# Kernel tuning notes

Hardware: AMD Instinct MI355X
Metric: run time of the kernel (lower is better)

## Reference

```python
import jax, jax.numpy as jnp
import numpy as np

B, S, E = 4, 2048, 1024
H, DK = 16, 64

def setup_inputs() -> dict:
    key = jax.random.key(0)
    ks = jax.random.split(key, 9)
    sc = 1.0 / np.sqrt(E)
    return {
        "q": jax.random.normal(ks[0], (B, S, E), jnp.float32),
        "Wq": jax.random.normal(ks[1], (E, H * DK), jnp.float32) * sc,
        "bq": jax.random.normal(ks[2], (H * DK,), jnp.float32) * 0.01,
        "Wk": jax.random.normal(ks[3], (E, H * DK), jnp.float32) * sc,
        "bk": jax.random.normal(ks[4], (H * DK,), jnp.float32) * 0.01,
        "Wv": jax.random.normal(ks[5], (E, H * DK), jnp.float32) * sc,
        "bv": jax.random.normal(ks[6], (H * DK,), jnp.float32) * 0.01,
        "Wo": jax.random.normal(ks[7], (H * DK, E), jnp.float32) * sc,
        "bo": jax.random.normal(ks[8], (E,), jnp.float32) * 0.01,
    }

def _split_heads(x):
    # (B, S, H*DK) -> (B, H, S, DK)
    return x.reshape(B, S, H, DK).transpose(0, 2, 1, 3)

def reference(q, Wq, bq, Wk, bk, Wv, bv, Wo, bo):
    # self-attention: k = v = q (torch module path when k=v=None)
    qh = _split_heads(q @ Wq + bq)
    kh = _split_heads(q @ Wk + bk)
    vh = _split_heads(q @ Wv + bv)
    scale = 1.0 / jnp.sqrt(jnp.asarray(DK, qh.dtype))
    scores = jnp.einsum("bhqd,bhkd->bhqk", qh, kh) * scale  # (B,H,S,S)
    attn = jax.nn.softmax(scores, axis=-1)
    ctx = jnp.einsum("bhqk,bhkd->bhqd", attn, vh)
    ctx = ctx.transpose(0, 2, 1, 3).reshape(B, S, H * DK)
    return ctx @ Wo + bo
```

## Files before the change

kernel.cpp:

```cpp
#include <hip/hip_runtime.h>
#include <hip/hip_bf16.h>
#include <math.h>


typedef _Float16 f16x8 __attribute__((ext_vector_type(8)));
typedef _Float16 f16x4 __attribute__((ext_vector_type(4)));
typedef _Float16 f16x2 __attribute__((ext_vector_type(2)));
typedef float    f32x4 __attribute__((ext_vector_type(4)));

#define MFMA16(a,b,c) __builtin_amdgcn_mfma_f32_16x16x32_f16(a,b,c,0,0,0)

__device__ __forceinline__ void async_cp16(const _Float16* g, _Float16* l) {
    __builtin_amdgcn_global_load_lds(
        (const __attribute__((address_space(1))) unsigned int*)g,
        (__attribute__((address_space(3))) unsigned int*)l,
        16, 0, 0);
}

__device__ __forceinline__ f16x2 pk(float a, float b) {
    return __builtin_bit_cast(f16x2, __builtin_amdgcn_cvt_pkrtz(a, b));
}

__global__ void __launch_bounds__(256) prep_weights(
    const float* __restrict__ Wq, const float* __restrict__ Wk,
    const float* __restrict__ Wv, const float* __restrict__ Wo,
    _Float16* __restrict__ wt)
{
    __shared__ float tile[32][33];
    int mat = blockIdx.y;
    const float* W = (mat==0)?Wq:(mat==1)?Wk:(mat==2)?Wv:Wo;
    _Float16* WT = wt + (size_t)mat*1048576;
    int t = blockIdx.x;
    int kb = (t & 31) * 32;
    int nb = (t >> 5) * 32;
    int tx = threadIdx.x & 31, ty = threadIdx.x >> 5;
    #pragma unroll
    for (int r = 0; r < 4; ++r) {
        int row = ty + r*8;
        tile[row][tx] = W[(size_t)(kb+row)*1024 + nb + tx];
    }
    __syncthreads();
    #pragma unroll
    for (int r = 0; r < 4; ++r) {
        int row = ty + r*8;
        WT[(size_t)(nb+row)*1024 + kb + tx] = (_Float16)tile[tx][row];
    }
}

__global__ void __launch_bounds__(256) cvt_x(
    const float* __restrict__ X, _Float16* __restrict__ Xh)
{
    int i = (blockIdx.x*256 + threadIdx.x)*4;
    f32x4 x = *(const f32x4*)&X[i];
    f16x4 h;
    #pragma unroll
    for (int k=0;k<4;k++) h[k] = (_Float16)x[k];
    *(f16x4*)&Xh[i] = h;
}

__global__ void __launch_bounds__(256) gemm_qkv(
    const _Float16* __restrict__ Xh, const _Float16* __restrict__ wt,
    const float* __restrict__ bq, const float* __restrict__ bk, const float* __restrict__ bv,
    _Float16* __restrict__ Q, _Float16* __restrict__ K, _Float16* __restrict__ Vt)
{
    __shared__ __align__(16) _Float16 sA[8192];
    __shared__ __align__(16) _Float16 sB[8192];

    const int id = blockIdx.x;
    const int msub = id & 7;
    const int t2 = id >> 3;
    const int nblk = t2 % 24;
    const int mblk = (t2 / 24) * 8 + msub;

    const int tid = threadIdx.x;
    const int wave = tid >> 6, lane = tid & 63;
    const int wr = wave >> 1, wc = wave & 1;
    const int q4 = lane >> 4, cc = lane & 15;

    const int mat = nblk >> 3;
    const int colbase = (nblk & 7) * 128;
    const _Float16* Bg = wt + (size_t)mat*1048576 + (size_t)colbase*1024;
    const _Float16* Ag = Xh + (size_t)mblk*131072;

    f32x4 acc[4][4] = {};

    const int srow = tid >> 3;
    const int scg  = ((tid & 7) ^ ((tid >> 3) & 7)) * 8;

    for (int kb = 0; kb < 1024; kb += 64) {
        __syncthreads();
        #pragma unroll
        for (int rr = 0; rr < 4; ++rr) {
            async_cp16(&Ag[(size_t)(rr*32 + srow)*1024 + kb + scg], sA + rr*2048 + wave*512);
            async_cp16(&Bg[(size_t)(rr*32 + srow)*1024 + kb + scg], sB + rr*2048 + wave*512);
        }
        __syncthreads();
        #pragma unroll
        for (int ks = 0; ks < 2; ++ks) {
            f16x8 af[4], bf[4];
            #pragma unroll
            for (int i=0;i<4;i++){
                af[i] = *(const f16x8*)&sA[(wr*64+i*16+cc)*64 + ((ks*4+q4)^(cc&7))*8];
                bf[i] = *(const f16x8*)&sB[(wc*64+i*16+cc)*64 + ((ks*4+q4)^(cc&7))*8];
            }
            #pragma unroll
            for (int i=0;i<4;i++)
                #pragma unroll
                for (int j=0;j<4;j++)
                    acc[i][j] = MFMA16(af[i], bf[j], acc[i][j]);
        }
    }

    const float* bias = (mat==0)?bq:(mat==1)?bk:bv;
    const float QSCALE = 0.125f * 1.44269504f;
    #pragma unroll
    for (int i=0;i<4;i++)
      #pragma unroll
      for (int j=0;j<4;j++)
        #pragma unroll
        for (int r=0;r<4;r++){
            int m = mblk*128 + wr*64 + i*16 + q4*4 + r;
            int ncol = colbase + wc*64 + j*16 + cc;
            float val = acc[i][j][r] + bias[ncol];
            int b = m >> 11, s = m & 2047;
            int h = ncol >> 6, dk = ncol & 63;
            if (mat == 2) {
                Vt[((size_t)(b*16+h)*64 + dk)*2048 + s] = (_Float16)val;
            } else {
                size_t qi = ((size_t)(b*16+h)*2048 + s)*64 + dk;
                if (mat == 0) Q[qi] = (_Float16)(val * QSCALE);
                else          K[qi] = (_Float16)val;
            }
        }
}

__global__ void __launch_bounds__(256,2) attn(
    const _Float16* __restrict__ Qg, const _Float16* __restrict__ Kg,
    const _Float16* __restrict__ Vg,
    _Float16* __restrict__ Ctx)
{
    __shared__ __align__(16) _Float16 sK[128][72];
    __shared__ __align__(16) _Float16 sV[64][136];
    __shared__ __align__(16) _Float16 sP[128*128];

    const int id = blockIdx.x;
    const int xcd = id & 7;
    const int t2 = id >> 3;
    const int qc = t2 & 15;
    const int bh = (t2 >> 4) * 8 + xcd;

    const int tid = threadIdx.x;
    const int wave = tid >> 6, lane = tid & 63;
    const int q4 = lane >> 4, cc = lane & 15;

    const size_t hoff = (size_t)bh * 131072;
    const _Float16* Qp = Qg + hoff;
    const _Float16* Kp = Kg + hoff;
    const _Float16* Vp = Vg + hoff;

    const int qbase = qc*128 + wave*32;

    f16x8 qf[2][2];
    #pragma unroll
    for (int m=0;m<2;m++)
      #pragma unroll
      for (int ks=0;ks<2;ks++)
        qf[m][ks] = *(const f16x8*)&Qp[(qbase+m*16+cc)*64 + ks*32 + q4*8];

    f16x8 vones;
    #pragma unroll
    for (int k=0;k<8;k++) vones[k] = (_Float16)1.0f;

    f32x4 o[2][4] = {};
    f32x4 oL[2] = {};

    const int r0 = tid >> 3, c8 = (tid & 7)*8;
    const int vrow = tid >> 4, vg = (tid & 15)*8;

    const int prow_w0 = wave*32 + cc;

    f16x8 kr[4], vr[4];
    #pragma unroll
    for (int p=0;p<4;p++){
        kr[p] = *(const f16x8*)&Kp[(p*32 + r0)*64 + c8];
        vr[p] = *(const f16x8*)&Vp[(size_t)(p*16 + vrow)*2048 + vg];
    }

    for (int kt = 0; kt < 16; ++kt) {
        __syncthreads();
        #pragma unroll
        for (int p=0;p<4;p++){
            *(f16x8*)&sK[p*32+r0][c8] = kr[p];
            *(f16x8*)&sV[p*16+vrow][vg] = vr[p];
        }
        __syncthreads();
        if (kt < 15) {
            #pragma unroll
            for (int p=0;p<4;p++){
                kr[p] = *(const f16x8*)&Kp[((kt+1)*128 + p*32 + r0)*64 + c8];
                vr[p] = *(const f16x8*)&Vp[(size_t)(p*16 + vrow)*2048 + (kt+1)*128 + vg];
            }
        }

        #pragma unroll
        for (int kj=0;kj<8;kj++){
            f16x8 k0 = *(const f16x8*)&sK[kj*16+cc][q4*8];
            f16x8 k1 = *(const f16x8*)&sK[kj*16+cc][32+q4*8];
            #pragma unroll
            for (int m=0;m<2;m++){
                f32x4 z = {};
                f32x4 s = MFMA16(k0, qf[m][0], z);
                s = MFMA16(k1, qf[m][1], s);
                float p0 = __builtin_amdgcn_exp2f(s[0]);
                float p1 = __builtin_amdgcn_exp2f(s[1]);
                float p2 = __builtin_amdgcn_exp2f(s[2]);
                float p3 = __builtin_amdgcn_exp2f(s[3]);
                union { f16x4 v4; f16x2 v2[2]; } u;
                u.v2[0] = pk(p0, p1);
                u.v2[1] = pk(p2, p3);
                int row = prow_w0 + m*16;
                int g   = (kj*2 + (q4>>1)) ^ (row & 7);
                *(f16x4*)&sP[row*128 + g*8 + (q4&1)*4] = u.v4;
            }
        }

        #pragma unroll
        for (int ks=0;ks<4;ks++){
            int g0 = ks*4 + q4;
            int row0 = prow_w0;
            int row1 = prow_w0 + 16;
            f16x8 p0 = *(const f16x8*)&sP[row0*128 + (g0 ^ (row0 & 7))*8];
            f16x8 p1 = *(const f16x8*)&sP[row1*128 + (g0 ^ (row1 & 7))*8];
            #pragma unroll
            for (int v=0;v<4;v++){
                f16x8 vf = *(const f16x8*)&sV[v*16+cc][ks*32+q4*8];
                o[0][v] = MFMA16(p0, vf, o[0][v]);
                o[1][v] = MFMA16(p1, vf, o[1][v]);
            }
            oL[0] = MFMA16(p0, vones, oL[0]);
            oL[1] = MFMA16(p1, vones, oL[1]);
        }
    }

    int b = bh >> 4, h = bh & 15;
    #pragma unroll
    for (int m=0;m<2;m++)
      #pragma unroll
      for (int r=0;r<4;r++){
        float inv = 1.f / oL[m][r];
        int s = qbase + m*16 + q4*4 + r;
        #pragma unroll
        for (int v=0;v<4;v++){
            float val = o[m][v][r]*inv;
            int dk = v*16 + cc;
            Ctx[((size_t)(b*2048+s)*16 + h)*64 + dk] = (_Float16)val;
        }
      }
}

__global__ void __launch_bounds__(256) gemm_out(
    const _Float16* __restrict__ Ctx, const _Float16* __restrict__ wt,
    const float* __restrict__ bo,
    float* __restrict__ out)
{
    __shared__ __align__(16) _Float16 sA[8192];
    __shared__ __align__(16) _Float16 sB[8192];

    const int id = blockIdx.x;
    const int msub = id & 7;
    const int t2 = id >> 3;
    const int nblk = t2 & 7;
    const int mblk = (t2 >> 3) * 8 + msub;

    const int tid = threadIdx.x;
    const int wave = tid >> 6, lane = tid & 63;
    const int wr = wave >> 1, wc = wave & 1;
    const int q4 = lane >> 4, cc = lane & 15;

    const _Float16* Bg = wt + (size_t)3*1048576 + (size_t)nblk*128*1024;
    const _Float16* Ag = Ctx + (size_t)mblk*131072;

    f32x4 acc[4][4] = {};
    const int srow = tid >> 3;
    const int scg  = ((tid & 7) ^ ((tid >> 3) & 7)) * 8;

    for (int kb = 0; kb < 1024; kb += 64) {
        __syncthreads();
        #pragma unroll
        for (int rr = 0; rr < 4; ++rr) {
            async_cp16(&Ag[(size_t)(rr*32 + srow)*1024 + kb + scg], sA + rr*2048 + wave*512);
            async_cp16(&Bg[(size_t)(rr*32 + srow)*1024 + kb + scg], sB + rr*2048 + wave*512);
        }
        __syncthreads();
        #pragma unroll
        for (int ks = 0; ks < 2; ++ks) {
            f16x8 af[4], bf[4];
            #pragma unroll
            for (int i=0;i<4;i++){
                af[i] = *(const f16x8*)&sA[(wr*64+i*16+cc)*64 + ((ks*4+q4)^(cc&7))*8];
                bf[i] = *(const f16x8*)&sB[(wc*64+i*16+cc)*64 + ((ks*4+q4)^(cc&7))*8];
            }
            #pragma unroll
            for (int i=0;i<4;i++)
                #pragma unroll
                for (int j=0;j<4;j++)
                    acc[i][j] = MFMA16(af[i], bf[j], acc[i][j]);
        }
    }

    #pragma unroll
    for (int i=0;i<4;i++)
      #pragma unroll
      for (int j=0;j<4;j++)
        #pragma unroll
        for (int r=0;r<4;r++){
            int m = mblk*128 + wr*64 + i*16 + q4*4 + r;
            int n = nblk*128 + wc*64 + j*16 + cc;
            out[(size_t)m*1024 + n] = acc[i][j][r] + bo[n];
        }
}

extern "C" void kernel_launch(void* const* d_in, const int* in_sizes, int n_in,
                              void* d_out, int out_size, void* d_ws, size_t ws_size,
                              hipStream_t stream)
{
    const float* q  = (const float*)d_in[0];
    const float* Wq = (const float*)d_in[1];
    const float* bq = (const float*)d_in[2];
    const float* Wk = (const float*)d_in[3];
    const float* bk = (const float*)d_in[4];
    const float* Wv = (const float*)d_in[5];
    const float* bv = (const float*)d_in[6];
    const float* Wo = (const float*)d_in[7];
    const float* bo = (const float*)d_in[8];
    float* out = (float*)d_out;

    _Float16* ws  = (_Float16*)d_ws;
    _Float16* wt  = ws;
    _Float16* Xh  = ws + 4194304;
    _Float16* Q   = ws + 12582912;
    _Float16* K   = ws + 20971520;
    _Float16* Vt  = ws + 29360128;
    _Float16* Ctx = Xh;

    prep_weights<<<dim3(1024,4), 256, 0, stream>>>(Wq, Wk, Wv, Wo, wt);
    cvt_x<<<dim3(8192), 256, 0, stream>>>(q, Xh);
    gemm_qkv<<<dim3(1536), 256, 0, stream>>>(Xh, wt, bq, bk, bv, Q, K, Vt);
    attn<<<dim3(1024), 256, 0, stream>>>(Q, K, Vt, Ctx);
    gemm_out<<<dim3(512), 256, 0, stream>>>(Ctx, wt, bo, out);
}
```

Measured before the change: 306.0 us.

## Keep softmax probabilities in registers via permlane swaps instead of LDS round-trip

The attention kernel no longer writes the exponentiated score tile to a shared-memory P buffer and reads it back. The S accumulator layout is converted into the A-operand layout of the PV MFMA with permlane32/permlane16 swaps. The row sum is now accumulated in fp32 registers and reduced across lanes, replacing the extra MFMA against a vector of ones. Freeing 32KB of LDS allows the launch bound to request 4 blocks per CU instead of 2, at the risk of register pressure and of errors in the permutation mapping.

```diff
diff --git a/kernel.cpp b/kernel.cpp
--- a/kernel.cpp
+++ b/kernel.cpp
@@ -7,6 +7,8 @@
 typedef _Float16 f16x4 __attribute__((ext_vector_type(4)));
 typedef _Float16 f16x2 __attribute__((ext_vector_type(2)));
 typedef float    f32x4 __attribute__((ext_vector_type(4)));
+typedef unsigned int u32x2 __attribute__((ext_vector_type(2)));
+typedef unsigned int u32x4 __attribute__((ext_vector_type(4)));
 
 #define MFMA16(a,b,c) __builtin_amdgcn_mfma_f32_16x16x32_f16(a,b,c,0,0,0)
 
@@ -134,14 +136,13 @@
         }
 }
 
-__global__ void __launch_bounds__(256,2) attn(
+__global__ void __launch_bounds__(256,4) attn(
     const _Float16* __restrict__ Qg, const _Float16* __restrict__ Kg,
     const _Float16* __restrict__ Vg,
     _Float16* __restrict__ Ctx)
 {
     __shared__ __align__(16) _Float16 sK[128][72];
     __shared__ __align__(16) _Float16 sV[64][136];
-    __shared__ __align__(16) _Float16 sP[128*128];
 
     const int id = blockIdx.x;
     const int xcd = id & 7;
@@ -167,17 +168,11 @@
       for (int ks=0;ks<2;ks++)
         qf[m][ks] = *(const f16x8*)&Qp[(qbase+m*16+cc)*64 + ks*32 + q4*8];
 
-    f16x8 vones;
-    #pragma unroll
-    for (int k=0;k<8;k++) vones[k] = (_Float16)1.0f;
-
     f32x4 o[2][4] = {};
-    f32x4 oL[2] = {};
+    float lsum[2] = {0.f, 0.f};
 
     const int r0 = tid >> 3, c8 = (tid & 7)*8;
     const int vrow = tid >> 4, vg = (tid & 15)*8;
-
-    const int prow_w0 = wave*32 + cc;
 
     f16x8 kr[4], vr[4];
     #pragma unroll
@@ -203,51 +198,68 @@
         }
 
         #pragma unroll
-        for (int kj=0;kj<8;kj++){
-            f16x8 k0 = *(const f16x8*)&sK[kj*16+cc][q4*8];
-            f16x8 k1 = *(const f16x8*)&sK[kj*16+cc][32+q4*8];
+        for (int ks=0;ks<4;ks++){
+            unsigned Ud[2][2], Wd[2][2];
+            #pragma unroll
+            for (int aa=0;aa<2;aa++){
+                int kj = ks*2 + aa;
+                f16x8 k0 = *(const f16x8*)&sK[kj*16+cc][q4*8];
+                f16x8 k1 = *(const f16x8*)&sK[kj*16+cc][32+q4*8];
+                #pragma unroll
+                for (int m=0;m<2;m++){
+                    f32x4 z = {};
+                    f32x4 s = MFMA16(k0, qf[m][0], z);
+                    s = MFMA16(k1, qf[m][1], s);
+                    float p0 = __builtin_amdgcn_exp2f(s[0]);
+                    float p1 = __builtin_amdgcn_exp2f(s[1]);
+                    float p2 = __builtin_amdgcn_exp2f(s[2]);
+                    float p3 = __builtin_amdgcn_exp2f(s[3]);
+                    lsum[m] += (p0 + p1) + (p2 + p3);
+                    unsigned d0 = __builtin_bit_cast(unsigned, pk(p0, p1));
+                    unsigned d1 = __builtin_bit_cast(unsigned, pk(p2, p3));
+                    if (aa == 0) { Ud[m][0] = d0; Ud[m][1] = d1; }
+                    else         { Wd[m][0] = d0; Wd[m][1] = d1; }
+                }
+            }
+            f16x8 pa[2];
             #pragma unroll
             for (int m=0;m<2;m++){
-                f32x4 z = {};
-                f32x4 s = MFMA16(k0, qf[m][0], z);
-                s = MFMA16(k1, qf[m][1], s);
-                float p0 = __builtin_amdgcn_exp2f(s[0]);
-                float p1 = __builtin_amdgcn_exp2f(s[1]);
-                float p2 = __builtin_amdgcn_exp2f(s[2]);
-                float p3 = __builtin_amdgcn_exp2f(s[3]);
-                union { f16x4 v4; f16x2 v2[2]; } u;
-                u.v2[0] = pk(p0, p1);
-                u.v2[1] = pk(p2, p3);
-                int row = prow_w0 + m*16;
-                int g   = (kj*2 + (q4>>1)) ^ (row & 7);
-                *(f16x4*)&sP[row*128 + g*8 + (q4&1)*4] = u.v4;
-            }
-        }
-
-        #pragma unroll
-        for (int ks=0;ks<4;ks++){
-            int g0 = ks*4 + q4;
-            int row0 = prow_w0;
-            int row1 = prow_w0 + 16;
-            f16x8 p0 = *(const f16x8*)&sP[row0*128 + (g0 ^ (row0 & 7))*8];
-            f16x8 p1 = *(const f16x8*)&sP[row1*128 + (g0 ^ (row1 & 7))*8];
+                u32x2 x0 = __builtin_amdgcn_permlane32_swap(Ud[m][0], Wd[m][0], false, false);
+                u32x2 r02 = __builtin_amdgcn_permlane16_swap(x0[0], x0[1], false, false);
+                u32x2 x1 = __builtin_amdgcn_permlane32_swap(Ud[m][1], Wd[m][1], false, false);
+                u32x2 r13 = __builtin_amdgcn_permlane16_swap(x1[0], x1[1], false, false);
+                u32x4 pw;
+                pw[0] = r02[0]; pw[1] = r13[0]; pw[2] = r02[1]; pw[3] = r13[1];
+                pa[m] = __builtin_bit_cast(f16x8, pw);
+            }
             #pragma unroll
             for (int v=0;v<4;v++){
                 f16x8 vf = *(const f16x8*)&sV[v*16+cc][ks*32+q4*8];
-                o[0][v] = MFMA16(p0, vf, o[0][v]);
-                o[1][v] = MFMA16(p1, vf, o[1][v]);
-            }
-            oL[0] = MFMA16(p0, vones, oL[0]);
-            oL[1] = MFMA16(p1, vones, oL[1]);
-        }
-    }
+                o[0][v] = MFMA16(pa[0], vf, o[0][v]);
+                o[1][v] = MFMA16(pa[1], vf, o[1][v]);
+            }
+        }
+    }
+
+    #pragma unroll
+    for (int m=0;m<2;m++){
+        lsum[m] += __shfl_xor(lsum[m], 16, 64);
+        lsum[m] += __shfl_xor(lsum[m], 32, 64);
+    }
+    __syncthreads();
+    float* sL = (float*)&sK[0][0];
+    if (q4 == 0) {
+        sL[wave*32 + cc]      = lsum[0];
+        sL[wave*32 + 16 + cc] = lsum[1];
+    }
+    __syncthreads();
 
     int b = bh >> 4, h = bh & 15;
     #pragma unroll
     for (int m=0;m<2;m++)
       #pragma unroll
       for (int r=0;r<4;r++){
-        float inv = 1.f / oL[m][r];
+        float inv = 1.f / sL[wave*32 + m*16 + q4*4 + r];
         int s = qbase + m*16 + q4*4 + r;
         #pragma unroll
         for (int v=0;v<4;v++){
```

Measured after the change: 351.2 us. 1.15x slower.
